# Kernel optimization log

Measured on AMD Instinct MI355X. Metric: run time of the kernel, lower is better.

The kernel has to match this reference:

```python
import jax, jax.numpy as jnp
import numpy as np

# Model dims (from MambaLayer: Mamba2(d_model=256, d_state=128, d_conv=4, expand=2, headdim=64))
D_MODEL = 256
D_INNER = 512
D_STATE = 128
NHEADS = 8
HEADDIM = 64
D_CONV = 4
CONV_DIM = D_INNER + 2 * D_STATE          # 768
D_IN_PROJ = 2 * D_INNER + 2 * D_STATE + NHEADS  # 1288
ATT_HEADS = 8
MLP_HID = 4 * D_MODEL
NUM_CLASSES = 2


def _mamba2(x, in_proj_w, conv_w, conv_b, dt_bias, A_log, D_param, norm_w, out_proj_w):
    """Mamba2 forward (SSD selective scan), ngroups=1, no in_proj/out_proj bias."""
    b, L, _ = x.shape
    zxbcdt = x @ in_proj_w.T                                   # (b,L,1288)
    z = zxbcdt[..., :D_INNER]                                   # gate
    xBC = zxbcdt[..., D_INNER:D_INNER + CONV_DIM]
    dt = jax.nn.softplus(zxbcdt[..., -NHEADS:] + dt_bias)       # (b,L,h)
    # depthwise causal conv1d (kernel 4) + SiLU
    xpad = jnp.pad(xBC, ((0, 0), (D_CONV - 1, 0), (0, 0)))
    xBC = sum(conv_w[:, k] * xpad[:, k:k + L, :] for k in range(D_CONV)) + conv_b
    xBC = jax.nn.silu(xBC)
    xs = xBC[..., :D_INNER].reshape(b, L, NHEADS, HEADDIM)      # (b,L,h,p)
    Bm = xBC[..., D_INNER:D_INNER + D_STATE]                    # (b,L,n)
    Cm = xBC[..., D_INNER + D_STATE:]                           # (b,L,n)
    dA = jnp.exp(dt * (-jnp.exp(A_log)))                        # (b,L,h)

    def step(h_prev, inp):
        dA_t, dt_t, B_t, C_t, x_t = inp                         # (b,h),(b,h),(b,n),(b,n),(b,h,p)
        h = h_prev * dA_t[..., None, None] + (dt_t[..., None] * x_t)[..., None] * B_t[:, None, None, :]
        return h, jnp.einsum('bhpn,bn->bhp', h, C_t)

    tfirst = lambda a: jnp.moveaxis(a, 1, 0)
    h0 = jnp.zeros((b, NHEADS, HEADDIM, D_STATE), x.dtype)
    _, ys = jax.lax.scan(step, h0, (tfirst(dA), tfirst(dt), tfirst(Bm), tfirst(Cm), tfirst(xs)))
    y = jnp.moveaxis(ys, 0, 1) + D_param[None, None, :, None] * xs
    # gated RMSNorm then out projection
    y = y.reshape(b, L, D_INNER) * jax.nn.silu(z)
    y = y * jax.lax.rsqrt(jnp.mean(y * y, -1, keepdims=True) + 1e-5) * norm_w
    return y @ out_proj_w.T


def _cross_attn(x, ctx, wq, wk, wv, wo, wo_b, w1, b1, ln_w, ln_b, w2, b2):
    """CrossModalAttention.forward: attn -> out_proj -> Mlp (no residual, per source)."""
    b, t, c = x.shape
    hd = c // ATT_HEADS
    heads = lambda a: a.reshape(b, -1, ATT_HEADS, hd).transpose(0, 2, 1, 3)
    q, k, v = heads(x @ wq.T), heads(ctx @ wk.T), heads(ctx @ wv.T)
    att = jax.nn.softmax(jnp.einsum('bhxd,bhyd->bhxy', q, k) * (hd ** -0.5), axis=-1)
    o = jnp.einsum('bhxy,bhyd->bhxd', att, v).transpose(0, 2, 1, 3).reshape(b, t, c)
    o = o @ wo.T + wo_b
    h = jax.nn.gelu(o @ w1.T + b1, approximate=False)
    mu = jnp.mean(h, -1, keepdims=True)
    var = jnp.mean((h - mu) ** 2, -1, keepdims=True)
    h = (h - mu) * jax.lax.rsqrt(var + 1e-5) * ln_w + ln_b
    return h @ w2.T + b2


def setup_inputs() -> dict:
    key = jax.random.key(0)
    ks = iter(jax.random.split(key, 32))
    f32 = jnp.float32
    w = lambda *s: jax.random.normal(next(ks), s, f32) * 0.02
    return {
        'x': jax.random.normal(next(ks), (2, 2048, D_MODEL), f32),
        'context': jax.random.normal(next(ks), (2, 2048, D_MODEL), f32),
        'in_proj_w': w(D_IN_PROJ, D_MODEL),
        'conv_w': w(CONV_DIM, D_CONV),
        'conv_b': jnp.zeros((CONV_DIM,), f32),
        'dt_bias': jax.random.normal(next(ks), (NHEADS,), f32) * 0.5,
        'A_log': jnp.log(jnp.linspace(1.0, 16.0, NHEADS).astype(f32)),
        'D_param': jnp.ones((NHEADS,), f32),
        'norm_w': jnp.ones((D_INNER,), f32),
        'out_proj_w': w(D_MODEL, D_INNER),
        'wq': w(D_MODEL, D_MODEL),
        'wk': w(D_MODEL, D_MODEL),
        'wv': w(D_MODEL, D_MODEL),
        'wo': w(D_MODEL, D_MODEL),
        'wo_b': jnp.zeros((D_MODEL,), f32),
        'w1': w(MLP_HID, D_MODEL),
        'b1': jnp.zeros((MLP_HID,), f32),
        'ln_w': jnp.ones((MLP_HID,), f32),
        'ln_b': jnp.zeros((MLP_HID,), f32),
        'w2': w(D_MODEL, MLP_HID),
        'b2': jnp.zeros((D_MODEL,), f32),
        'head_w': w(NUM_CLASSES, D_MODEL),
        'head_b': jnp.zeros((NUM_CLASSES,), f32),
    }


def reference(x, context, in_proj_w, conv_w, conv_b, dt_bias, A_log, D_param, norm_w, out_proj_w,
              wq, wk, wv, wo, wo_b, w1, b1, ln_w, ln_b, w2, b2, head_w, head_b):
    h = x + _mamba2(x, in_proj_w, conv_w, conv_b, dt_bias, A_log, D_param, norm_w, out_proj_w)
    h = _cross_attn(h, context, wq, wk, wv, wo, wo_b, w1, b1, ln_w, ln_b, w2, b2)
    # ClsHead: mean-pool over tokens, linear to classes
    return jnp.mean(h, axis=1) @ head_w.T + head_b
```

## Files before the change

### kernel.cpp

```cpp
#include <hip/hip_runtime.h>
#include <hip/hip_bf16.h>
#include <math.h>

#define DEVFN __device__ __forceinline__

constexpr int BATCH = 2;
constexpr int SEQ   = 2048;
constexpr int DM    = 256;
constexpr int DI    = 512;
constexpr int DSTATE= 128;
constexpr int NH    = 8;
constexpr int HD    = 64;
constexpr int CDIM  = 768;
constexpr int DPROJ = 1288;
constexpr int MTOK  = BATCH*SEQ;
constexpr int HID   = 1024;
constexpr int CHUNK = 32;
constexpr int NCHUNK= SEQ/CHUNK;
constexpr int NSPLIT= 4;
constexpr int KVLEN = SEQ/NSPLIT;

typedef __bf16 bf16x8 __attribute__((ext_vector_type(8)));
typedef __bf16 bf16x4 __attribute__((ext_vector_type(4)));
typedef float  f32x4  __attribute__((ext_vector_type(4)));

DEVFN float gelu_exact(float x){ return 0.5f*x*(1.f+erff(x*0.70710678118654752f)); }
DEVFN float silu_f(float x){ return x/(1.f+expf(-x)); }

DEVFN bf16x8 pack8(float4 a, float4 b){
  bf16x8 r;
  r[0]=(__bf16)a.x; r[1]=(__bf16)a.y; r[2]=(__bf16)a.z; r[3]=(__bf16)a.w;
  r[4]=(__bf16)b.x; r[5]=(__bf16)b.y; r[6]=(__bf16)b.z; r[7]=(__bf16)b.w;
  return r;
}
DEVFN f32x4 mfma16(bf16x8 a, bf16x8 b, f32x4 c){
  return __builtin_amdgcn_mfma_f32_16x16x32_bf16(a, b, c, 0, 0, 0);
}

__global__ __launch_bounds__(256)
void cvt_in(const float* __restrict__ x, const float* __restrict__ ctx,
            __bf16* __restrict__ xbf, __bf16* __restrict__ ctxbf)
{
  const int MN = MTOK*DM;
  int idx = (blockIdx.x*256 + threadIdx.x)*4;
  const float* src = (idx < MN) ? (x + idx) : (ctx + idx - MN);
  __bf16* dst = (idx < MN) ? (xbf + idx) : (ctxbf + idx - MN);
  float4 v = *(const float4*)src;
  bf16x4 o;
  o[0]=(__bf16)v.x; o[1]=(__bf16)v.y; o[2]=(__bf16)v.z; o[3]=(__bf16)v.w;
  *(bf16x4*)dst = o;
}

template<int ACT, bool HASBIAS>
__global__ __launch_bounds__(256)
void gemm128(const __bf16* __restrict__ A, const float* __restrict__ W,
             const float* __restrict__ bias, __bf16* __restrict__ C,
             int M, int N, int K)
{
  __shared__ __bf16 As[128][40];
  __shared__ __bf16 Ws[128][40];
  const int tid = threadIdx.x;
  const int bm = blockIdx.x * 128, bn = blockIdx.y * 128;
  const int wv = tid >> 6, lane = tid & 63;
  const int quad = lane >> 4, mr = lane & 15;
  const int wm = (wv >> 1) * 64, wn = (wv & 1) * 64;
  const int srow = tid >> 2;
  const int skc  = (tid & 3) * 8;

  const __bf16* ap0 = A + (size_t)(bm + srow)*K + skc;
  const __bf16* ap1 = A + (size_t)(bm + srow + 64)*K + skc;
  const bool wok0 = (bn + srow) < N;
  const bool wok1 = (bn + srow + 64) < N;
  const float* wp0 = W + (size_t)(bn + srow)*K + skc;
  const float* wp1 = W + (size_t)(bn + srow + 64)*K + skc;

  bf16x8 A0 = *(const bf16x8*)ap0;
  bf16x8 A1 = *(const bf16x8*)ap1;
  float4 z4 = make_float4(0,0,0,0);
  float4 W00 = wok0 ? *(const float4*)wp0     : z4;
  float4 W01 = wok0 ? *(const float4*)(wp0+4) : z4;
  float4 W10 = wok1 ? *(const float4*)wp1     : z4;
  float4 W11 = wok1 ? *(const float4*)(wp1+4) : z4;

  f32x4 acc[4][4];
  #pragma unroll
  for (int i=0;i<4;i++)
    #pragma unroll
    for (int j=0;j<4;j++) acc[i][j] = f32x4{0.f,0.f,0.f,0.f};

  for (int k0 = 0; k0 < K; k0 += 32) {
    __syncthreads();
    *(bf16x8*)&As[srow   ][skc] = A0;
    *(bf16x8*)&As[srow+64][skc] = A1;
    *(bf16x8*)&Ws[srow   ][skc] = pack8(W00, W01);
    *(bf16x8*)&Ws[srow+64][skc] = pack8(W10, W11);
    __syncthreads();
    if (k0 + 32 < K){
      int kn = k0 + 32;
      A0 = *(const bf16x8*)(ap0+kn);
      A1 = *(const bf16x8*)(ap1+kn);
      W00 = wok0 ? *(const float4*)(wp0+kn)   : z4;
      W01 = wok0 ? *(const float4*)(wp0+kn+4) : z4;
      W10 = wok1 ? *(const float4*)(wp1+kn)   : z4;
      W11 = wok1 ? *(const float4*)(wp1+kn+4) : z4;
    }
    bf16x8 af[4], bf[4];
    #pragma unroll
    for (int i=0;i<4;i++) af[i] = *(const bf16x8*)&As[wm + i*16 + mr][quad*8];
    #pragma unroll
    for (int j=0;j<4;j++) bf[j] = *(const bf16x8*)&Ws[wn + j*16 + mr][quad*8];
    #pragma unroll
    for (int i=0;i<4;i++)
      #pragma unroll
      for (int j=0;j<4;j++)
        acc[i][j] = mfma16(af[i], bf[j], acc[i][j]);
  }

  #pragma unroll
  for (int j=0;j<4;j++){
    int col = bn + wn + j*16 + mr;
    if (col >= N) continue;
    float bb = HASBIAS ? bias[col] : 0.f;
    #pragma unroll
    for (int i=0;i<4;i++){
      #pragma unroll
      for (int reg=0; reg<4; reg++){
        int row = bm + wm + i*16 + quad*4 + reg;
        float vv = acc[i][j][reg] + bb;
        if (ACT == 1) vv = gelu_exact(vv);
        C[(size_t)row*N + col] = (__bf16)vv;
      }
    }
  }
}

template<int EPI, bool HASBIAS, bool HASRES>
__global__ __launch_bounds__(256)
void gemm64d(const __bf16* __restrict__ A, const float* __restrict__ W,
             const float* __restrict__ bias, const __bf16* __restrict__ resid,
             float* __restrict__ Cf, __bf16* __restrict__ Cb,
             int M, int N, int K)
{
  __shared__ __bf16 As[64][40];
  __shared__ __bf16 Ws[64][40];
  const int tid = threadIdx.x;
  const int bm = blockIdx.x*64, bn = blockIdx.y*64;
  const int w = tid >> 6, lane = tid & 63;
  const int quad = lane >> 4, mr = lane & 15;
  const int wm = (w >> 1) * 32, wn = (w & 1) * 32;
  const int srow = tid >> 2, skc = (tid & 3) * 8;

  const __bf16* ap = A + (size_t)(bm + srow)*K + skc;
  const float*  wp = W + (size_t)(bn + srow)*K + skc;
  bf16x8 a0 = *(const bf16x8*)ap;
  float4 w0 = *(const float4*)wp, w1 = *(const float4*)(wp+4);

  f32x4 acc[2][2];
  #pragma unroll
  for (int i=0;i<2;i++)
    #pragma unroll
    for (int j=0;j<2;j++) acc[i][j] = f32x4{0.f,0.f,0.f,0.f};

  for (int k0 = 0; k0 < K; k0 += 32){
    __syncthreads();
    *(bf16x8*)&As[srow][skc] = a0;
    *(bf16x8*)&Ws[srow][skc] = pack8(w0, w1);
    __syncthreads();
    if (k0 + 32 < K){
      a0 = *(const bf16x8*)(ap+k0+32);
      w0 = *(const float4*)(wp+k0+32); w1 = *(const float4*)(wp+k0+36);
    }
    bf16x8 af[2], bfr[2];
    af[0]  = *(const bf16x8*)&As[wm      + mr][quad*8];
    af[1]  = *(const bf16x8*)&As[wm + 16 + mr][quad*8];
    bfr[0] = *(const bf16x8*)&Ws[wn      + mr][quad*8];
    bfr[1] = *(const bf16x8*)&Ws[wn + 16 + mr][quad*8];
    #pragma unroll
    for (int i=0;i<2;i++)
      #pragma unroll
      for (int j=0;j<2;j++)
        acc[i][j] = mfma16(af[i], bfr[j], acc[i][j]);
  }

  #pragma unroll
  for (int j=0;j<2;j++){
    int col = bn + wn + j*16 + mr;
    float bb = HASBIAS ? bias[col] : 0.f;
    #pragma unroll
    for (int i=0;i<2;i++)
      #pragma unroll
      for (int reg=0;reg<4;reg++){
        int row = bm + wm + i*16 + quad*4 + reg;
        float vv = acc[i][j][reg] + bb;
        if (HASRES) vv += (float)resid[(size_t)row*N + col];
        if (EPI == 0) Cf[(size_t)row*N + col] = vv;
        else          Cb[(size_t)row*N + col] = (__bf16)vv;
      }
  }
}

__global__ __launch_bounds__(256)
void qkv_gemm(const __bf16* __restrict__ hres, const __bf16* __restrict__ ctx,
              const float* __restrict__ wq, const float* __restrict__ wk,
              const float* __restrict__ wv, __bf16* __restrict__ qo,
              __bf16* __restrict__ ko, __bf16* __restrict__ vt)
{
  __shared__ __bf16 As[64][40];
  __shared__ __bf16 Ws[64][40];
  const int tid = threadIdx.x;
  const int bm = blockIdx.x*64, bn = blockIdx.y*64, z = blockIdx.z;
  const int K = DM, N = DM;
  const __bf16* A = (z == 0) ? hres : ctx;
  const float*  W = (z == 0) ? wq : (z == 1) ? wk : wv;
  const int w = tid >> 6, lane = tid & 63;
  const int quad = lane >> 4, mr = lane & 15;
  const int wm = (w >> 1) * 32, wn = (w & 1) * 32;
  const int srow = tid >> 2, skc = (tid & 3) * 8;

  const __bf16* ap = A + (size_t)(bm + srow)*K + skc;
  const float*  wp = W + (size_t)(bn + srow)*K + skc;
  bf16x8 a0 = *(const bf16x8*)ap;
  float4 w0 = *(const float4*)wp, w1 = *(const float4*)(wp+4);

  f32x4 acc[2][2];
  #pragma unroll
  for (int i=0;i<2;i++)
    #pragma unroll
    for (int j=0;j<2;j++) acc[i][j] = f32x4{0.f,0.f,0.f,0.f};

  for (int k0 = 0; k0 < K; k0 += 32){
    __syncthreads();
    *(bf16x8*)&As[srow][skc] = a0;
    *(bf16x8*)&Ws[srow][skc] = pack8(w0, w1);
    __syncthreads();
    if (k0 + 32 < K){
      a0 = *(const bf16x8*)(ap+k0+32);
      w0 = *(const float4*)(wp+k0+32); w1 = *(const float4*)(wp+k0+36);
    }
    bf16x8 af[2], bfr[2];
    af[0]  = *(const bf16x8*)&As[wm      + mr][quad*8];
    af[1]  = *(const bf16x8*)&As[wm + 16 + mr][quad*8];
    bfr[0] = *(const bf16x8*)&Ws[wn      + mr][quad*8];
    bfr[1] = *(const bf16x8*)&Ws[wn + 16 + mr][quad*8];
    #pragma unroll
    for (int i=0;i<2;i++)
      #pragma unroll
      for (int j=0;j<2;j++)
        acc[i][j] = mfma16(af[i], bfr[j], acc[i][j]);
  }

  if (z < 2){
    __bf16* C = (z == 0) ? qo : ko;
    #pragma unroll
    for (int j=0;j<2;j++){
      int col = bn + wn + j*16 + mr;
      #pragma unroll
      for (int i=0;i<2;i++)
        #pragma unroll
        for (int reg=0;reg<4;reg++){
          int row = bm + wm + i*16 + quad*4 + reg;
          C[(size_t)row*N + col] = (__bf16)acc[i][j][reg];
        }
    }
  } else {
    #pragma unroll
    for (int j=0;j<2;j++){
      int col = bn + wn + j*16 + mr;
      int h = col >> 5, dl = col & 31;
      #pragma unroll
      for (int i=0;i<2;i++){
        int rowb = bm + wm + i*16 + quad*4;
        int b = rowb >> 11, t = rowb & 2047;
        bf16x4 o;
        #pragma unroll
        for (int reg=0;reg<4;reg++) o[reg] = (__bf16)acc[i][j][reg];
        *(bf16x4*)(vt + ((size_t)(b*NH + h)*32 + dl)*SEQ + t) = o;
      }
    }
  }
}

__global__ __launch_bounds__(256)
void dtda_kernel(const __bf16* __restrict__ zx, const float* __restrict__ dt_bias,
                 const float* __restrict__ A_log, float* __restrict__ dtb,
                 float* __restrict__ ldab)
{
  int idx = blockIdx.x*256 + threadIdx.x;
  int t = idx & 2047, bh = idx >> 11;
  int b = bh >> 3, h = bh & 7;
  float raw = (float)zx[(size_t)(b*SEQ + t)*DPROJ + 2*DI + 2*DSTATE + h] + dt_bias[h];
  float dt = fmaxf(raw, 0.f) + log1pf(expf(-fabsf(raw)));
  dtb[idx]  = dt;
  ldab[idx] = -__expf(A_log[h]) * dt;
}

__global__ __launch_bounds__(256)
void conv_silu_kernel(const __bf16* __restrict__ zx, const float* __restrict__ convw,
                      const float* __restrict__ convb, __bf16* __restrict__ xBC)
{
  int idx = blockIdx.x*256 + threadIdx.x;
  int c = idx % CDIM;
  int bt = idx / CDIM;
  int b = bt >> 11, t = bt & 2047;
  float4 w4 = *(const float4*)(convw + c*4);
  const float* wp = (const float*)&w4;
  float acc = convb[c];
  #pragma unroll
  for (int k=0;k<4;k++){
    int ts = t - 3 + k;
    if (ts >= 0)
      acc = fmaf(wp[k], (float)zx[(size_t)(b*SEQ + ts)*DPROJ + DI + c], acc);
  }
  xBC[(size_t)bt*CDIM + c] = (__bf16)silu_f(acc);
}

__global__ __launch_bounds__(256)
void chunk_state(const __bf16* __restrict__ xBC, const float* __restrict__ dtb,
                 const float* __restrict__ ldab, __bf16* __restrict__ Hc,
                 float* __restrict__ Ac)
{
  const int blk = blockIdx.x;
  const int ch = blk & 63, bh = blk >> 6;
  const int b = bh >> 3, h = bh & 7;
  const int t0 = ch*CHUNK;
  const int tid = threadIdx.x;
  __shared__ float csS[CHUNK], wendS[CHUNK];
  __shared__ __bf16 Xw[64][40];
  __shared__ __bf16 Bt[128][40];

  if (tid < 32){
    float v  = ldab[bh*SEQ + t0 + tid];
    float dtv = dtb[bh*SEQ + t0 + tid];
    #pragma unroll
    for (int off=1; off<32; off<<=1){
      float o = __shfl_up(v, off, 32);
      if (tid >= off) v += o;
    }
    csS[tid] = v;
    float cs31 = __shfl(v, 31, 32);
    wendS[tid] = __expf(cs31 - v) * dtv;
  }
  __syncthreads();
  {
    int s  = tid >> 3;
    int pg = (tid & 7) * 8;
    bf16x8 xv = *(const bf16x8*)(xBC + (size_t)(b*SEQ + t0 + s)*CDIM + h*HD + pg);
    float wgt = wendS[s];
    #pragma unroll
    for (int e=0;e<8;e++) Xw[pg+e][s] = (__bf16)((float)xv[e] * wgt);
    int ng = (tid & 7) * 16;
    const __bf16* bp = xBC + (size_t)(b*SEQ + t0 + s)*CDIM + DI + ng;
    bf16x8 b0 = *(const bf16x8*)bp;
    bf16x8 b1 = *(const bf16x8*)(bp+8);
    #pragma unroll
    for (int e=0;e<8;e++){ Bt[ng+e][s] = b0[e]; Bt[ng+8+e][s] = b1[e]; }
  }
  if (tid == 0) Ac[blk] = __expf(csS[31]);
  __syncthreads();

  const int w = tid >> 6, lane = tid & 63, quad = lane >> 4, mr = lane & 15;
  bf16x8 af = *(const bf16x8*)&Xw[w*16 + mr][quad*8];
  __bf16* out = Hc + (size_t)blk*8192;
  #pragma unroll
  for (int j=0;j<8;j++){
    bf16x8 bfm = *(const bf16x8*)&Bt[j*16 + mr][quad*8];
    f32x4 a = mfma16(af, bfm, f32x4{0.f,0.f,0.f,0.f});
    #pragma unroll
    for (int reg=0; reg<4; reg++){
      int p = w*16 + quad*4 + reg;
      out[p*128 + j*16 + mr] = (__bf16)a[reg];
    }
  }
}

__global__ __launch_bounds__(256)
void state_prefix(__bf16* __restrict__ Hc, const float* __restrict__ Ac)
{
  const int blk = blockIdx.x;
  const int bh = blk >> 5, pp = blk & 31;
  const int tid = threadIdx.x;
  const int p = pp*2 + (tid >> 7), n = tid & 127;
  __shared__ float AcS[64];
  if (tid < 64) AcS[tid] = Ac[bh*64 + tid];
  __syncthreads();
  __bf16* base = Hc + (size_t)bh*64*8192 + p*128 + n;
  float run = 0.f;
  float v = (float)base[0];
  for (int c=0; c<64; c++){
    float vn = (c < 63) ? (float)base[(size_t)(c+1)*8192] : 0.f;
    base[(size_t)c*8192] = (__bf16)run;
    run = fmaf(AcS[c], run, v);
    v = vn;
  }
}

__global__ __launch_bounds__(256)
void chunk_out(const __bf16* __restrict__ xBC, const float* __restrict__ dtb,
               const float* __restrict__ ldab, const __bf16* __restrict__ h0buf,
               const float* __restrict__ Dparam, __bf16* __restrict__ ybuf)
{
  const int blk = blockIdx.x;
  const int ch = blk & 63, bh = blk >> 6;
  const int b = bh >> 3, h = bh & 7;
  const int t0 = ch*CHUNK;
  const int tid = threadIdx.x;
  __shared__ float csS[CHUNK], dtS[CHUNK];
  __shared__ __bf16 Xct[64][40];
  __shared__ __bf16 Ms[32][40];

  if (tid < 32){
    float v = ldab[bh*SEQ + t0 + tid];
    dtS[tid] = dtb[bh*SEQ + t0 + tid];
    #pragma unroll
    for (int off=1; off<32; off<<=1){
      float o = __shfl_up(v, off, 32);
      if (tid >= off) v += o;
    }
    csS[tid] = v;
  }
  __syncthreads();
  {
    int s  = tid >> 3;
    int pg = (tid & 7) * 8;
    bf16x8 xv = *(const bf16x8*)(xBC + (size_t)(b*SEQ + t0 + s)*CDIM + h*HD + pg);
    #pragma unroll
    for (int e=0;e<8;e++) Xct[pg+e][s] = xv[e];
  }

  const int w = tid >> 6, lane = tid & 63, quad = lane >> 4, mr = lane & 15;
  const int ti = w >> 1, si = w & 1;

  const __bf16* Crow = xBC + (size_t)(b*SEQ + t0 + ti*16 + mr)*CDIM + DI + DSTATE;
  bf16x8 af[4];
  #pragma unroll
  for (int kk=0; kk<4; kk++)
    af[kk] = *(const bf16x8*)(Crow + kk*32 + quad*8);
  f32x4 sacc = f32x4{0.f,0.f,0.f,0.f};
  const __bf16* Brow = xBC + (size_t)(b*SEQ + t0 + si*16 + mr)*CDIM + DI;
  #pragma unroll
  for (int kk=0; kk<4; kk++){
    bf16x8 bfm = *(const bf16x8*)(Brow + kk*32 + quad*8);
    sacc = mfma16(af[kk], bfm, sacc);
  }
  #pragma unroll
  for (int reg=0; reg<4; reg++){
    int t = ti*16 + quad*4 + reg;
    int s = si*16 + mr;
    float m = 0.f;
    if (s <= t) m = __expf(csS[t] - csS[s]) * dtS[s] * sacc[reg];
    Ms[t][s] = (__bf16)m;
  }
  __syncthreads();

  f32x4 acc[2] = { f32x4{0.f,0.f,0.f,0.f}, f32x4{0.f,0.f,0.f,0.f} };
  const __bf16* h0r = h0buf + (size_t)blk*8192;
  #pragma unroll
  for (int j=0;j<2;j++){
    int p = (si*2 + j)*16 + mr;
    #pragma unroll
    for (int kk=0; kk<4; kk++){
      bf16x8 bh0 = *(const bf16x8*)(h0r + (size_t)p*128 + kk*32 + quad*8);
      acc[j] = mfma16(af[kk], bh0, acc[j]);
    }
  }
  #pragma unroll
  for (int reg=0;reg<4;reg++){
    int t = ti*16 + quad*4 + reg;
    float e = __expf(csS[t]);
    acc[0][reg] *= e;
    acc[1][reg] *= e;
  }
  bf16x8 am = *(const bf16x8*)&Ms[ti*16 + mr][quad*8];
  #pragma unroll
  for (int j=0;j<2;j++){
    int p = (si*2 + j)*16 + mr;
    bf16x8 bx = *(const bf16x8*)&Xct[p][quad*8];
    acc[j] = mfma16(am, bx, acc[j]);
  }
  const float Dv = Dparam[h];
  #pragma unroll
  for (int j=0;j<2;j++){
    int p = (si*2 + j)*16 + mr;
    #pragma unroll
    for (int reg=0;reg<4;reg++){
      int t = t0 + ti*16 + quad*4 + reg;
      float xv = (float)xBC[(size_t)(b*SEQ + t)*CDIM + h*HD + p];
      ybuf[(size_t)(b*SEQ + t)*DI + h*HD + p] = (__bf16)fmaf(Dv, xv, acc[j][reg]);
    }
  }
}

__global__ __launch_bounds__(128)
void rmsgate_kernel(__bf16* __restrict__ y, const __bf16* __restrict__ zx,
                    const float* __restrict__ normw)
{
  const int row = blockIdx.x, tid = threadIdx.x;
  const __bf16* zrow = zx + (size_t)row*DPROJ;
  __bf16* yrow = y + (size_t)row*DI;
  bf16x4 yv = *(const bf16x4*)(yrow + tid*4);
  bf16x4 zv = *(const bf16x4*)(zrow + tid*4);
  float g[4];
  float ss = 0.f;
  #pragma unroll
  for (int e=0;e<4;e++){
    g[e] = (float)yv[e] * silu_f((float)zv[e]);
    ss += g[e]*g[e];
  }
  #pragma unroll
  for (int off=1; off<64; off<<=1) ss += __shfl_xor(ss, off);
  __shared__ float red[2];
  if ((tid & 63)==0) red[tid>>6] = ss;
  __syncthreads();
  float tot = red[0] + red[1];
  float rs = rsqrtf(tot * (1.f/DI) + 1e-5f);
  float4 nw = *(const float4*)(normw + tid*4);
  const float* nwp = (const float*)&nw;
  bf16x4 o;
  #pragma unroll
  for (int e=0;e<4;e++) o[e] = (__bf16)(g[e]*rs*nwp[e]);
  *(bf16x4*)(yrow + tid*4) = o;
}

__global__ __launch_bounds__(256)
void flash_part(const __bf16* __restrict__ qb, const __bf16* __restrict__ kb,
                const __bf16* __restrict__ vt, float* __restrict__ opart,
                float* __restrict__ lpart)
{
  const int qt = blockIdx.x, ksp = blockIdx.y, bh = blockIdx.z;
  const int b = bh >> 3, h = bh & 7;
  const int tid = threadIdx.x;
  const int w = tid >> 6, lane = tid & 63;
  const int quad = lane >> 4, mr = lane & 15;
  const int qrow0 = b*SEQ + qt*128 + w*32;
  const float SC = 0.17677669529663687f;
  __shared__ __bf16 Pq[4][32][72];

  bf16x8 bq[2];
  #pragma unroll
  for (int i2=0;i2<2;i2++)
    bq[i2] = *(const bf16x8*)(qb + (size_t)(qrow0 + i2*16 + mr)*DM + h*32 + quad*8);

  f32x4 accO[2][2];
  #pragma unroll
  for (int i=0;i<2;i++)
    #pragma unroll
    for (int j=0;j<2;j++) accO[i][j] = f32x4{0.f,0.f,0.f,0.f};
  float lacc[2] = {0.f, 0.f};

  for (int kt=0; kt<KVLEN/64; kt++){
    const int kbase = b*SEQ + ksp*KVLEN + kt*64;
    float tl[2] = {0.f, 0.f};
    #pragma unroll
    for (int ik=0; ik<4; ik++){
      bf16x8 ak = *(const bf16x8*)(kb + (size_t)(kbase + ik*16 + mr)*DM + h*32 + quad*8);
      #pragma unroll
      for (int jq=0; jq<2; jq++){
        f32x4 st = mfma16(ak, bq[jq], f32x4{0.f,0.f,0.f,0.f});
        bf16x4 e4;
        float sa = 0.f;
        #pragma unroll
        for (int reg=0; reg<4; reg++){
          float e = __expf(st[reg] * SC);
          sa += e;
          e4[reg] = (__bf16)e;
        }
        tl[jq] += sa;
        *(bf16x4*)&Pq[w][jq*16 + mr][ik*16 + quad*4] = e4;
      }
    }
    #pragma unroll
    for (int jq=0; jq<2; jq++){
      float v = tl[jq];
      v += __shfl_xor(v, 16);
      v += __shfl_xor(v, 32);
      lacc[jq] += v;
    }
    #pragma unroll
    for (int ks=0; ks<2; ks++){
      bf16x8 pa0 = *(const bf16x8*)&Pq[w][     mr][ks*32 + quad*8];
      bf16x8 pa1 = *(const bf16x8*)&Pq[w][16 + mr][ks*32 + quad*8];
      #pragma unroll
      for (int j2=0; j2<2; j2++){
        bf16x8 bv = *(const bf16x8*)(vt + ((size_t)bh*32 + j2*16 + mr)*SEQ
                        + ksp*KVLEN + kt*64 + ks*32 + quad*8);
        accO[0][j2] = mfma16(pa0, bv, accO[0][j2]);
        accO[1][j2] = mfma16(pa1, bv, accO[1][j2]);
      }
    }
  }

  #pragma unroll
  for (int i2=0;i2<2;i2++)
    #pragma unroll
    for (int j2=0;j2<2;j2++)
      #pragma unroll
      for (int reg=0;reg<4;reg++){
        int row = qrow0 + i2*16 + quad*4 + reg;
        opart[((size_t)ksp*MTOK + row)*DM + h*32 + j2*16 + mr] = accO[i2][j2][reg];
      }
  if (quad == 0){
    #pragma unroll
    for (int jq=0;jq<2;jq++)
      lpart[((size_t)ksp*16 + bh)*SEQ + (qt*128 + w*32 + jq*16 + mr)] = lacc[jq];
  }
}

__global__ __launch_bounds__(256)
void flash_combine(const float* __restrict__ opart, const float* __restrict__ lpart,
                   __bf16* __restrict__ o)
{
  int idx = blockIdx.x*256 + threadIdx.x;
  int row = idx >> 6, d4 = (idx & 63)*4;
  int h = d4 >> 5;
  int b = row >> 11, t = row & 2047;
  float sx=0.f, sy=0.f, sz=0.f, sw=0.f, lsum=0.f;
  #pragma unroll
  for (int s4=0; s4<NSPLIT; s4++){
    float4 vv = *(const float4*)(opart + ((size_t)s4*MTOK + row)*DM + d4);
    sx += vv.x; sy += vv.y; sz += vv.z; sw += vv.w;
    lsum += lpart[((size_t)s4*16 + b*8 + h)*SEQ + t];
  }
  float inv = 1.f / lsum;
  bf16x4 ov;
  ov[0]=(__bf16)(sx*inv); ov[1]=(__bf16)(sy*inv);
  ov[2]=(__bf16)(sz*inv); ov[3]=(__bf16)(sw*inv);
  *(bf16x4*)(o + (size_t)row*DM + d4) = ov;
}

__global__ __launch_bounds__(256)
void lnorm_kernel(__bf16* __restrict__ hb, const float* __restrict__ lnw,
                  const float* __restrict__ lnb)
{
  const int row = blockIdx.x, tid = threadIdx.x;
  __bf16* hr = hb + (size_t)row*HID;
  bf16x4 v4 = *(const bf16x4*)(hr + tid*4);
  float v[4];
  float sum = 0.f, sq = 0.f;
  #pragma unroll
  for (int e=0;e<4;e++){ v[e] = (float)v4[e]; sum += v[e]; sq += v[e]*v[e]; }
  #pragma unroll
  for (int off=1; off<64; off<<=1){ sum += __shfl_xor(sum,off); sq += __shfl_xor(sq,off); }
  __shared__ float s1[4], s2[4];
  int w = tid>>6;
  if ((tid & 63)==0){ s1[w]=sum; s2[w]=sq; }
  __syncthreads();
  sum = (s1[0]+s1[1])+(s1[2]+s1[3]);
  sq  = (s2[0]+s2[1])+(s2[2]+s2[3]);
  float mu = sum * (1.f/HID);
  float var = sq * (1.f/HID) - mu*mu;
  float rstd = rsqrtf(var + 1e-5f);
  float4 wv = *(const float4*)(lnw + tid*4);
  float4 bv = *(const float4*)(lnb + tid*4);
  const float* wp = (const float*)&wv;
  const float* bp = (const float*)&bv;
  bf16x4 o;
  #pragma unroll
  for (int e=0;e<4;e++) o[e] = (__bf16)((v[e]-mu)*rstd*wp[e] + bp[e]);
  *(bf16x4*)(hr + tid*4) = o;
}

__global__ __launch_bounds__(256)
void pool_partial(const float* __restrict__ h2, float* __restrict__ part)
{
  const int blk = blockIdx.x;
  const int b = blk >> 4, seg = blk & 15;
  const int tid = threadIdx.x;
  float s = 0.f;
  const float* base = h2 + ((size_t)b*SEQ + seg*128)*DM + tid;
  #pragma unroll 8
  for (int t=0; t<128; t++) s += base[(size_t)t*DM];
  part[((size_t)b*16 + seg)*DM + tid] = s;
}

__global__ __launch_bounds__(128)
void head_kernel(const float* __restrict__ part, const float* __restrict__ headw,
                 const float* __restrict__ headb, float* __restrict__ out)
{
  const int b = blockIdx.x;
  const int tid = threadIdx.x;
  __shared__ float pooled[DM];
  for (int c=tid; c<DM; c+=128){
    float s = 0.f;
    #pragma unroll
    for (int gidx=0; gidx<16; gidx++) s += part[((size_t)b*16 + gidx)*DM + c];
    pooled[c] = s * (1.f/SEQ);
  }
  __syncthreads();
  int cls = tid >> 6, lane = tid & 63;
  float acc = 0.f;
  for (int c=lane; c<DM; c+=64) acc += pooled[c]*headw[cls*DM + c];
  #pragma unroll
  for (int off=1; off<64; off<<=1) acc += __shfl_xor(acc, off);
  if (lane == 0) out[b*2 + cls] = acc + headb[cls];
}

extern "C" void kernel_launch(void* const* d_in, const int* in_sizes, int n_in,
                              void* d_out, int out_size, void* d_ws, size_t ws_size,
                              hipStream_t stream)
{
  const float* x         = (const float*)d_in[0];
  const float* context   = (const float*)d_in[1];
  const float* in_proj_w = (const float*)d_in[2];
  const float* conv_w    = (const float*)d_in[3];
  const float* conv_b    = (const float*)d_in[4];
  const float* dt_bias   = (const float*)d_in[5];
  const float* A_log     = (const float*)d_in[6];
  const float* D_param   = (const float*)d_in[7];
  const float* norm_w    = (const float*)d_in[8];
  const float* out_proj_w= (const float*)d_in[9];
  const float* wq  = (const float*)d_in[10];
  const float* wk  = (const float*)d_in[11];
  const float* wv  = (const float*)d_in[12];
  const float* wo  = (const float*)d_in[13];
  const float* wo_b= (const float*)d_in[14];
  const float* w1  = (const float*)d_in[15];
  const float* b1  = (const float*)d_in[16];
  const float* ln_w= (const float*)d_in[17];
  const float* ln_b= (const float*)d_in[18];
  const float* w2  = (const float*)d_in[19];
  const float* b2  = (const float*)d_in[20];
  const float* head_w = (const float*)d_in[21];
  const float* head_b = (const float*)d_in[22];
  float* out = (float*)d_out;
  float* ws  = (float*)d_ws;

  __bf16* xbf   = (__bf16*)ws;
  __bf16* ctxbf = (__bf16*)(ws + 524288);
  __bf16* zx    = (__bf16*)(ws + 1048576);
  __bf16* xBC   = (__bf16*)(ws + 3686400);
  float* dtb    = ws + 5259264;
  float* ldab   = ws + 5292032;
  __bf16* Hcb   = (__bf16*)(ws + 5324800);
  float* Acb    = ws + 9519104;
  __bf16* ybuf  = (__bf16*)(ws + 9520128);
  __bf16* hres  = (__bf16*)(ws + 10568704);
  __bf16* qbf   = (__bf16*)(ws + 11092992);
  __bf16* kbf   = (__bf16*)(ws + 11617280);
  __bf16* vtbf  = (__bf16*)(ws + 12141568);
  float* opart  = ws + 12665856;
  float* lpart  = ws + 16860160;
  __bf16* obf   = (__bf16*)(ws + 16991232);
  __bf16* o2bf  = (__bf16*)(ws + 17515520);
  __bf16* h1bf  = (__bf16*)(ws + 5324800);
  float* h2     = ws + 12665856;
  float* partb  = ws + 16860160;

  const dim3 g64(MTOK/64, DM/64);

  cvt_in<<<dim3(2*MTOK*DM/1024), dim3(256), 0, stream>>>(x, context, xbf, ctxbf);
  gemm128<0,false><<<dim3(MTOK/128, (DPROJ+127)/128), dim3(256), 0, stream>>>(
      xbf, in_proj_w, nullptr, zx, MTOK, DPROJ, DM);
  dtda_kernel<<<dim3(MTOK*NH/256), dim3(256), 0, stream>>>(zx, dt_bias, A_log, dtb, ldab);
  conv_silu_kernel<<<dim3(MTOK*CDIM/256), dim3(256), 0, stream>>>(
      zx, conv_w, conv_b, xBC);
  chunk_state<<<dim3(BATCH*NH*NCHUNK), dim3(256), 0, stream>>>(
      xBC, dtb, ldab, Hcb, Acb);
  state_prefix<<<dim3(BATCH*NH*32), dim3(256), 0, stream>>>(Hcb, Acb);
  chunk_out<<<dim3(BATCH*NH*NCHUNK), dim3(256), 0, stream>>>(
      xBC, dtb, ldab, Hcb, D_param, ybuf);
  rmsgate_kernel<<<dim3(MTOK), dim3(128), 0, stream>>>(ybuf, zx, norm_w);
  gemm64d<1,false,true><<<g64, dim3(256), 0, stream>>>(
      ybuf, out_proj_w, nullptr, xbf, nullptr, hres, MTOK, DM, DI);
  qkv_gemm<<<dim3(MTOK/64, DM/64, 3), dim3(256), 0, stream>>>(
      hres, ctxbf, wq, wk, wv, qbf, kbf, vtbf);
  flash_part<<<dim3(SEQ/128, NSPLIT, BATCH*NH), dim3(256), 0, stream>>>(
      qbf, kbf, vtbf, opart, lpart);
  flash_combine<<<dim3(MTOK*64/256), dim3(256), 0, stream>>>(opart, lpart, obf);
  gemm64d<1,true,false><<<g64, dim3(256), 0, stream>>>(
      obf, wo, wo_b, nullptr, nullptr, o2bf, MTOK, DM, DM);
  gemm128<1,true><<<dim3(MTOK/128, HID/128), dim3(256), 0, stream>>>(
      o2bf, w1, b1, h1bf, MTOK, HID, DM);
  lnorm_kernel<<<dim3(MTOK), dim3(256), 0, stream>>>(h1bf, ln_w, ln_b);
  gemm64d<0,true,false><<<g64, dim3(256), 0, stream>>>(
      h1bf, w2, b2, nullptr, h2, nullptr, MTOK, DM, HID);
  pool_partial<<<dim3(32), dim3(256), 0, stream>>>(h2, partb);
  head_kernel<<<dim3(BATCH), dim3(128), 0, stream>>>(partb, head_w, head_b, out);
  (void)in_sizes; (void)n_in; (void)out_size; (void)ws_size;
}
```

Before: 309.9 us.

## Fuse input conversion, dt, flash combine into neighbors; pool before final linear

```diff
diff --git a/kernel.cpp b/kernel.cpp
--- a/kernel.cpp
+++ b/kernel.cpp
@@ -22,6 +22,7 @@
 
 typedef __bf16 bf16x8 __attribute__((ext_vector_type(8)));
 typedef __bf16 bf16x4 __attribute__((ext_vector_type(4)));
+typedef __bf16 bf16x2 __attribute__((ext_vector_type(2)));
 typedef float  f32x4  __attribute__((ext_vector_type(4)));
 
 DEVFN float gelu_exact(float x){ return 0.5f*x*(1.f+erff(x*0.70710678118654752f)); }
@@ -37,23 +38,9 @@
   return __builtin_amdgcn_mfma_f32_16x16x32_bf16(a, b, c, 0, 0, 0);
 }
 
-__global__ __launch_bounds__(256)
-void cvt_in(const float* __restrict__ x, const float* __restrict__ ctx,
-            __bf16* __restrict__ xbf, __bf16* __restrict__ ctxbf)
-{
-  const int MN = MTOK*DM;
-  int idx = (blockIdx.x*256 + threadIdx.x)*4;
-  const float* src = (idx < MN) ? (x + idx) : (ctx + idx - MN);
-  __bf16* dst = (idx < MN) ? (xbf + idx) : (ctxbf + idx - MN);
-  float4 v = *(const float4*)src;
-  bf16x4 o;
-  o[0]=(__bf16)v.x; o[1]=(__bf16)v.y; o[2]=(__bf16)v.z; o[3]=(__bf16)v.w;
-  *(bf16x4*)dst = o;
-}
-
-template<int ACT, bool HASBIAS>
-__global__ __launch_bounds__(256)
-void gemm128(const __bf16* __restrict__ A, const float* __restrict__ W,
+template<int ACT, bool HASBIAS, bool AF32>
+__global__ __launch_bounds__(256)
+void gemm128(const void* __restrict__ Av, const float* __restrict__ W,
              const float* __restrict__ bias, __bf16* __restrict__ C,
              int M, int N, int K)
 {
@@ -67,15 +54,23 @@
   const int srow = tid >> 2;
   const int skc  = (tid & 3) * 8;
 
-  const __bf16* ap0 = A + (size_t)(bm + srow)*K + skc;
-  const __bf16* ap1 = A + (size_t)(bm + srow + 64)*K + skc;
+  const float*  af0 = (const float*)Av + (size_t)(bm + srow)*K + skc;
+  const float*  af1 = (const float*)Av + (size_t)(bm + srow + 64)*K + skc;
+  const __bf16* ab0 = (const __bf16*)Av + (size_t)(bm + srow)*K + skc;
+  const __bf16* ab1 = (const __bf16*)Av + (size_t)(bm + srow + 64)*K + skc;
   const bool wok0 = (bn + srow) < N;
   const bool wok1 = (bn + srow + 64) < N;
   const float* wp0 = W + (size_t)(bn + srow)*K + skc;
   const float* wp1 = W + (size_t)(bn + srow + 64)*K + skc;
 
-  bf16x8 A0 = *(const bf16x8*)ap0;
-  bf16x8 A1 = *(const bf16x8*)ap1;
+  bf16x8 A0, A1;
+  if (AF32){
+    A0 = pack8(*(const float4*)af0, *(const float4*)(af0+4));
+    A1 = pack8(*(const float4*)af1, *(const float4*)(af1+4));
+  } else {
+    A0 = *(const bf16x8*)ab0;
+    A1 = *(const bf16x8*)ab1;
+  }
   float4 z4 = make_float4(0,0,0,0);
   float4 W00 = wok0 ? *(const float4*)wp0     : z4;
   float4 W01 = wok0 ? *(const float4*)(wp0+4) : z4;
@@ -97,23 +92,28 @@
     __syncthreads();
     if (k0 + 32 < K){
       int kn = k0 + 32;
-      A0 = *(const bf16x8*)(ap0+kn);
-      A1 = *(const bf16x8*)(ap1+kn);
+      if (AF32){
+        A0 = pack8(*(const float4*)(af0+kn), *(const float4*)(af0+kn+4));
+        A1 = pack8(*(const float4*)(af1+kn), *(const float4*)(af1+kn+4));
+      } else {
+        A0 = *(const bf16x8*)(ab0+kn);
+        A1 = *(const bf16x8*)(ab1+kn);
+      }
       W00 = wok0 ? *(const float4*)(wp0+kn)   : z4;
       W01 = wok0 ? *(const float4*)(wp0+kn+4) : z4;
       W10 = wok1 ? *(const float4*)(wp1+kn)   : z4;
       W11 = wok1 ? *(const float4*)(wp1+kn+4) : z4;
     }
-    bf16x8 af[4], bf[4];
-    #pragma unroll
-    for (int i=0;i<4;i++) af[i] = *(const bf16x8*)&As[wm + i*16 + mr][quad*8];
-    #pragma unroll
-    for (int j=0;j<4;j++) bf[j] = *(const bf16x8*)&Ws[wn + j*16 + mr][quad*8];
+    bf16x8 afr[4], bfr[4];
+    #pragma unroll
+    for (int i=0;i<4;i++) afr[i] = *(const bf16x8*)&As[wm + i*16 + mr][quad*8];
+    #pragma unroll
+    for (int j=0;j<4;j++) bfr[j] = *(const bf16x8*)&Ws[wn + j*16 + mr][quad*8];
     #pragma unroll
     for (int i=0;i<4;i++)
       #pragma unroll
       for (int j=0;j<4;j++)
-        acc[i][j] = mfma16(af[i], bf[j], acc[i][j]);
+        acc[i][j] = mfma16(afr[i], bfr[j], acc[i][j]);
   }
 
   #pragma unroll
@@ -134,12 +134,10 @@
   }
 }
 
-template<int EPI, bool HASBIAS, bool HASRES>
-__global__ __launch_bounds__(256)
-void gemm64d(const __bf16* __restrict__ A, const float* __restrict__ W,
-             const float* __restrict__ bias, const __bf16* __restrict__ resid,
-             float* __restrict__ Cf, __bf16* __restrict__ Cb,
-             int M, int N, int K)
+__global__ __launch_bounds__(256)
+void gemm_outproj(const __bf16* __restrict__ A, const float* __restrict__ W,
+                  const float* __restrict__ residf, __bf16* __restrict__ Cb,
+                  int M, int N, int K)
 {
   __shared__ __bf16 As[64][40];
   __shared__ __bf16 Ws[64][40];
@@ -185,22 +183,19 @@
   #pragma unroll
   for (int j=0;j<2;j++){
     int col = bn + wn + j*16 + mr;
-    float bb = HASBIAS ? bias[col] : 0.f;
     #pragma unroll
     for (int i=0;i<2;i++)
       #pragma unroll
       for (int reg=0;reg<4;reg++){
         int row = bm + wm + i*16 + quad*4 + reg;
-        float vv = acc[i][j][reg] + bb;
-        if (HASRES) vv += (float)resid[(size_t)row*N + col];
-        if (EPI == 0) Cf[(size_t)row*N + col] = vv;
-        else          Cb[(size_t)row*N + col] = (__bf16)vv;
+        float vv = acc[i][j][reg] + residf[(size_t)row*N + col];
+        Cb[(size_t)row*N + col] = (__bf16)vv;
       }
   }
 }
 
 __global__ __launch_bounds__(256)
-void qkv_gemm(const __bf16* __restrict__ hres, const __bf16* __restrict__ ctx,
+void qkv_gemm(const __bf16* __restrict__ hres, const float* __restrict__ ctx,
               const float* __restrict__ wq, const float* __restrict__ wk,
               const float* __restrict__ wv, __bf16* __restrict__ qo,
               __bf16* __restrict__ ko, __bf16* __restrict__ vt)
@@ -210,16 +205,19 @@
   const int tid = threadIdx.x;
   const int bm = blockIdx.x*64, bn = blockIdx.y*64, z = blockIdx.z;
   const int K = DM, N = DM;
-  const __bf16* A = (z == 0) ? hres : ctx;
+  const bool abf = (z == 0);
   const float*  W = (z == 0) ? wq : (z == 1) ? wk : wv;
   const int w = tid >> 6, lane = tid & 63;
   const int quad = lane >> 4, mr = lane & 15;
   const int wm = (w >> 1) * 32, wn = (w & 1) * 32;
   const int srow = tid >> 2, skc = (tid & 3) * 8;
 
-  const __bf16* ap = A + (size_t)(bm + srow)*K + skc;
-  const float*  wp = W + (size_t)(bn + srow)*K + skc;
-  bf16x8 a0 = *(const bf16x8*)ap;
+  const __bf16* apb = hres + (size_t)(bm + srow)*K + skc;
+  const float*  apf = ctx  + (size_t)(bm + srow)*K + skc;
+  const float*  wp  = W + (size_t)(bn + srow)*K + skc;
+  bf16x8 a0;
+  if (abf) a0 = *(const bf16x8*)apb;
+  else     a0 = pack8(*(const float4*)apf, *(const float4*)(apf+4));
   float4 w0 = *(const float4*)wp, w1 = *(const float4*)(wp+4);
 
   f32x4 acc[2][2];
@@ -234,7 +232,8 @@
     *(bf16x8*)&Ws[srow][skc] = pack8(w0, w1);
     __syncthreads();
     if (k0 + 32 < K){
-      a0 = *(const bf16x8*)(ap+k0+32);
+      if (abf) a0 = *(const bf16x8*)(apb+k0+32);
+      else     a0 = pack8(*(const float4*)(apf+k0+32), *(const float4*)(apf+k0+36));
       w0 = *(const float4*)(wp+k0+32); w1 = *(const float4*)(wp+k0+36);
     }
     bf16x8 af[2], bfr[2];
@@ -281,22 +280,89 @@
 }
 
 __global__ __launch_bounds__(256)
-void dtda_kernel(const __bf16* __restrict__ zx, const float* __restrict__ dt_bias,
-                 const float* __restrict__ A_log, float* __restrict__ dtb,
-                 float* __restrict__ ldab)
-{
-  int idx = blockIdx.x*256 + threadIdx.x;
-  int t = idx & 2047, bh = idx >> 11;
-  int b = bh >> 3, h = bh & 7;
-  float raw = (float)zx[(size_t)(b*SEQ + t)*DPROJ + 2*DI + 2*DSTATE + h] + dt_bias[h];
-  float dt = fmaxf(raw, 0.f) + log1pf(expf(-fabsf(raw)));
-  dtb[idx]  = dt;
-  ldab[idx] = -__expf(A_log[h]) * dt;
-}
-
-__global__ __launch_bounds__(256)
-void conv_silu_kernel(const __bf16* __restrict__ zx, const float* __restrict__ convw,
-                      const float* __restrict__ convb, __bf16* __restrict__ xBC)
+void wo_gemm(const float* __restrict__ opart, const float* __restrict__ lpart,
+             const float* __restrict__ W, const float* __restrict__ bias,
+             __bf16* __restrict__ Cb)
+{
+  __shared__ __bf16 As[64][40];
+  __shared__ __bf16 Ws[64][40];
+  const int tid = threadIdx.x;
+  const int bm = blockIdx.x*64, bn = blockIdx.y*64;
+  const int K = DM, N = DM;
+  const int w = tid >> 6, lane = tid & 63;
+  const int quad = lane >> 4, mr = lane & 15;
+  const int wm = (w >> 1) * 32, wn = (w & 1) * 32;
+  const int srow = tid >> 2, skc = (tid & 3) * 8;
+
+  const int row = bm + srow;
+  const int b = row >> 11, t = row & 2047;
+  const float* wp = W + (size_t)(bn + srow)*K + skc;
+
+  f32x4 acc[2][2];
+  #pragma unroll
+  for (int i=0;i<2;i++)
+    #pragma unroll
+    for (int j=0;j<2;j++) acc[i][j] = f32x4{0.f,0.f,0.f,0.f};
+
+  for (int k0 = 0; k0 < K; k0 += 32){
+    __syncthreads();
+    {
+      int col = k0 + skc;
+      int h = col >> 5;
+      float lsum = 0.f;
+      #pragma unroll
+      for (int s=0;s<NSPLIT;s++)
+        lsum += lpart[((size_t)s*16 + b*8 + h)*SEQ + t];
+      float inv = 1.f / lsum;
+      float va[8] = {0,0,0,0,0,0,0,0};
+      #pragma unroll
+      for (int s=0;s<NSPLIT;s++){
+        const float* op = opart + ((size_t)s*MTOK + row)*DM + col;
+        float4 u0 = *(const float4*)op;
+        float4 u1 = *(const float4*)(op+4);
+        va[0]+=u0.x; va[1]+=u0.y; va[2]+=u0.z; va[3]+=u0.w;
+        va[4]+=u1.x; va[5]+=u1.y; va[6]+=u1.z; va[7]+=u1.w;
+      }
+      bf16x8 a;
+      #pragma unroll
+      for (int e=0;e<8;e++) a[e] = (__bf16)(va[e]*inv);
+      *(bf16x8*)&As[srow][skc] = a;
+      float4 w0 = *(const float4*)(wp+k0);
+      float4 w1 = *(const float4*)(wp+k0+4);
+      *(bf16x8*)&Ws[srow][skc] = pack8(w0, w1);
+    }
+    __syncthreads();
+    bf16x8 af[2], bfr[2];
+    af[0]  = *(const bf16x8*)&As[wm      + mr][quad*8];
+    af[1]  = *(const bf16x8*)&As[wm + 16 + mr][quad*8];
+    bfr[0] = *(const bf16x8*)&Ws[wn      + mr][quad*8];
+    bfr[1] = *(const bf16x8*)&Ws[wn + 16 + mr][quad*8];
+    #pragma unroll
+    for (int i=0;i<2;i++)
+      #pragma unroll
+      for (int j=0;j<2;j++)
+        acc[i][j] = mfma16(af[i], bfr[j], acc[i][j]);
+  }
+
+  #pragma unroll
+  for (int j=0;j<2;j++){
+    int col = bn + wn + j*16 + mr;
+    float bb = bias[col];
+    #pragma unroll
+    for (int i=0;i<2;i++)
+      #pragma unroll
+      for (int reg=0;reg<4;reg++){
+        int r2 = bm + wm + i*16 + quad*4 + reg;
+        Cb[(size_t)r2*N + col] = (__bf16)(acc[i][j][reg] + bb);
+      }
+  }
+}
+
+__global__ __launch_bounds__(256)
+void conv_dt_kernel(const __bf16* __restrict__ zx, const float* __restrict__ convw,
+                    const float* __restrict__ convb, const float* __restrict__ dt_bias,
+                    const float* __restrict__ A_log, __bf16* __restrict__ xBC,
+                    float* __restrict__ dtb, float* __restrict__ ldab)
 {
   int idx = blockIdx.x*256 + threadIdx.x;
   int c = idx % CDIM;
@@ -312,6 +378,13 @@
       acc = fmaf(wp[k], (float)zx[(size_t)(b*SEQ + ts)*DPROJ + DI + c], acc);
   }
   xBC[(size_t)bt*CDIM + c] = (__bf16)silu_f(acc);
+  if (c < NH){
+    float raw = (float)zx[(size_t)bt*DPROJ + 2*DI + 2*DSTATE + c] + dt_bias[c];
+    float dt = fmaxf(raw, 0.f) + log1pf(expf(-fabsf(raw)));
+    int o = (b*NH + c)*SEQ + t;
+    dtb[o]  = dt;
+    ldab[o] = -__expf(A_log[c]) * dt;
+  }
 }
 
 __global__ __launch_bounds__(256)
@@ -377,20 +450,24 @@
 void state_prefix(__bf16* __restrict__ Hc, const float* __restrict__ Ac)
 {
   const int blk = blockIdx.x;
-  const int bh = blk >> 5, pp = blk & 31;
+  const int bh = blk >> 4, sub = blk & 15;
   const int tid = threadIdx.x;
-  const int p = pp*2 + (tid >> 7), n = tid & 127;
+  const int off = sub*512 + tid*2;
   __shared__ float AcS[64];
   if (tid < 64) AcS[tid] = Ac[bh*64 + tid];
+  __bf16* base = Hc + (size_t)bh*64*8192 + off;
+  bf16x2 v[64];
+  #pragma unroll
+  for (int c=0;c<64;c++) v[c] = *(const bf16x2*)(base + (size_t)c*8192);
   __syncthreads();
-  __bf16* base = Hc + (size_t)bh*64*8192 + p*128 + n;
-  float run = 0.f;
-  float v = (float)base[0];
-  for (int c=0; c<64; c++){
-    float vn = (c < 63) ? (float)base[(size_t)(c+1)*8192] : 0.f;
-    base[(size_t)c*8192] = (__bf16)run;
-    run = fmaf(AcS[c], run, v);
-    v = vn;
+  float r0 = 0.f, r1 = 0.f;
+  #pragma unroll
+  for (int c=0;c<64;c++){
+    bf16x2 o; o[0] = (__bf16)r0; o[1] = (__bf16)r1;
+    *(bf16x2*)(base + (size_t)c*8192) = o;
+    float a = AcS[c];
+    r0 = fmaf(a, r0, (float)v[c][0]);
+    r1 = fmaf(a, r1, (float)v[c][1]);
   }
 }
 
@@ -603,28 +680,6 @@
     for (int jq=0;jq<2;jq++)
       lpart[((size_t)ksp*16 + bh)*SEQ + (qt*128 + w*32 + jq*16 + mr)] = lacc[jq];
   }
-}
-
-__global__ __launch_bounds__(256)
-void flash_combine(const float* __restrict__ opart, const float* __restrict__ lpart,
-                   __bf16* __restrict__ o)
-{
-  int idx = blockIdx.x*256 + threadIdx.x;
-  int row = idx >> 6, d4 = (idx & 63)*4;
-  int h = d4 >> 5;
-  int b = row >> 11, t = row & 2047;
-  float sx=0.f, sy=0.f, sz=0.f, sw=0.f, lsum=0.f;
-  #pragma unroll
-  for (int s4=0; s4<NSPLIT; s4++){
-    float4 vv = *(const float4*)(opart + ((size_t)s4*MTOK + row)*DM + d4);
-    sx += vv.x; sy += vv.y; sz += vv.z; sw += vv.w;
-    lsum += lpart[((size_t)s4*16 + b*8 + h)*SEQ + t];
-  }
-  float inv = 1.f / lsum;
-  bf16x4 ov;
-  ov[0]=(__bf16)(sx*inv); ov[1]=(__bf16)(sy*inv);
-  ov[2]=(__bf16)(sz*inv); ov[3]=(__bf16)(sw*inv);
-  *(bf16x4*)(o + (size_t)row*DM + d4) = ov;
 }
 
 __global__ __launch_bounds__(256)
@@ -660,38 +715,62 @@
 }
 
 __global__ __launch_bounds__(256)
-void pool_partial(const float* __restrict__ h2, float* __restrict__ part)
+void pool_ln(const __bf16* __restrict__ h1, float* __restrict__ pp)
 {
   const int blk = blockIdx.x;
-  const int b = blk >> 4, seg = blk & 15;
+  const int b = blk >> 6, seg = blk & 63;
   const int tid = threadIdx.x;
-  float s = 0.f;
-  const float* base = h2 + ((size_t)b*SEQ + seg*128)*DM + tid;
-  #pragma unroll 8
-  for (int t=0; t<128; t++) s += base[(size_t)t*DM];
-  part[((size_t)b*16 + seg)*DM + tid] = s;
-}
-
-__global__ __launch_bounds__(128)
-void head_kernel(const float* __restrict__ part, const float* __restrict__ headw,
-                 const float* __restrict__ headb, float* __restrict__ out)
-{
-  const int b = blockIdx.x;
-  const int tid = threadIdx.x;
-  __shared__ float pooled[DM];
-  for (int c=tid; c<DM; c+=128){
-    float s = 0.f;
-    #pragma unroll
-    for (int gidx=0; gidx<16; gidx++) s += part[((size_t)b*16 + gidx)*DM + c];
-    pooled[c] = s * (1.f/SEQ);
+  const int c4 = tid*4;
+  float4 s = make_float4(0,0,0,0);
+  const __bf16* basep = h1 + ((size_t)(b*SEQ + seg*32))*HID + c4;
+  #pragma unroll 4
+  for (int r=0;r<32;r++){
+    bf16x4 v = *(const bf16x4*)(basep + (size_t)r*HID);
+    s.x += (float)v[0]; s.y += (float)v[1]; s.z += (float)v[2]; s.w += (float)v[3];
+  }
+  *(float4*)(pp + ((size_t)(b*64+seg))*HID + c4) = s;
+}
+
+__global__ __launch_bounds__(256)
+void head2_kernel(const float* __restrict__ pp, const float* __restrict__ w2,
+                  const float* __restrict__ b2, const float* __restrict__ hw,
+                  const float* __restrict__ hb, float* __restrict__ out)
+{
+  const int b = blockIdx.x, tid = threadIdx.x;
+  __shared__ float pooled[HID];
+  __shared__ float w2h[DM];
+  {
+    int c4 = tid*4;
+    float4 s = make_float4(0,0,0,0);
+    #pragma unroll 4
+    for (int seg=0;seg<64;seg++){
+      float4 v = *(const float4*)(pp + ((size_t)(b*64+seg))*HID + c4);
+      s.x+=v.x; s.y+=v.y; s.z+=v.z; s.w+=v.w;
+    }
+    const float inv = 1.f/(float)SEQ;
+    *(float4*)&pooled[c4] = make_float4(s.x*inv, s.y*inv, s.z*inv, s.w*inv);
   }
   __syncthreads();
-  int cls = tid >> 6, lane = tid & 63;
-  float acc = 0.f;
-  for (int c=lane; c<DM; c+=64) acc += pooled[c]*headw[cls*DM + c];
-  #pragma unroll
-  for (int off=1; off<64; off<<=1) acc += __shfl_xor(acc, off);
-  if (lane == 0) out[b*2 + cls] = acc + headb[cls];
+  {
+    float acc = 0.f;
+    const float* wr = w2 + (size_t)tid*HID;
+    #pragma unroll 8
+    for (int k=0;k<HID;k+=4){
+      float4 wv4 = *(const float4*)(wr+k);
+      float4 pv  = *(const float4*)&pooled[k];
+      acc += wv4.x*pv.x + wv4.y*pv.y + wv4.z*pv.z + wv4.w*pv.w;
+    }
+    w2h[tid] = acc + b2[tid];
+  }
+  __syncthreads();
+  if (tid < 128){
+    int cls = tid >> 6, lane = tid & 63;
+    float acc = 0.f;
+    for (int c=lane;c<DM;c+=64) acc += w2h[c]*hw[cls*DM+c];
+    #pragma unroll
+    for (int off=1;off<64;off<<=1) acc += __shfl_xor(acc, off);
+    if (lane == 0) out[b*2 + cls] = acc + hb[cls];
+  }
 }
 
 extern "C" void kernel_launch(void* const* d_in, const int* in_sizes, int n_in,
@@ -724,56 +803,47 @@
   float* out = (float*)d_out;
   float* ws  = (float*)d_ws;
 
-  __bf16* xbf   = (__bf16*)ws;
-  __bf16* ctxbf = (__bf16*)(ws + 524288);
-  __bf16* zx    = (__bf16*)(ws + 1048576);
-  __bf16* xBC   = (__bf16*)(ws + 3686400);
-  float* dtb    = ws + 5259264;
-  float* ldab   = ws + 5292032;
-  __bf16* Hcb   = (__bf16*)(ws + 5324800);
-  float* Acb    = ws + 9519104;
-  __bf16* ybuf  = (__bf16*)(ws + 9520128);
-  __bf16* hres  = (__bf16*)(ws + 10568704);
-  __bf16* qbf   = (__bf16*)(ws + 11092992);
-  __bf16* kbf   = (__bf16*)(ws + 11617280);
-  __bf16* vtbf  = (__bf16*)(ws + 12141568);
-  float* opart  = ws + 12665856;
-  float* lpart  = ws + 16860160;
-  __bf16* obf   = (__bf16*)(ws + 16991232);
-  __bf16* o2bf  = (__bf16*)(ws + 17515520);
-  __bf16* h1bf  = (__bf16*)(ws + 5324800);
-  float* h2     = ws + 12665856;
-  float* partb  = ws + 16860160;
+  __bf16* zx    = (__bf16*)ws;
+  __bf16* xBC   = (__bf16*)(ws + 2637824);
+  float* dtb    = ws + 4210688;
+  float* ldab   = ws + 4243456;
+  __bf16* Hcb   = (__bf16*)(ws + 4276224);
+  float* Acb    = ws + 8470528;
+  __bf16* ybuf  = (__bf16*)(ws + 8471552);
+  __bf16* hres  = (__bf16*)(ws + 9520128);
+  __bf16* qbf   = (__bf16*)(ws + 10044416);
+  __bf16* kbf   = (__bf16*)(ws + 10568704);
+  __bf16* vtbf  = (__bf16*)(ws + 11092992);
+  float* opart  = ws + 11617280;
+  float* lpart  = ws + 15811584;
+  __bf16* o2bf  = (__bf16*)(ws + 15942656);
+  __bf16* h1bf  = (__bf16*)(ws + 4276224);
+  float* poolp  = ws + 11617280;
 
   const dim3 g64(MTOK/64, DM/64);
 
-  cvt_in<<<dim3(2*MTOK*DM/1024), dim3(256), 0, stream>>>(x, context, xbf, ctxbf);
-  gemm128<0,false><<<dim3(MTOK/128, (DPROJ+127)/128), dim3(256), 0, stream>>>(
-      xbf, in_proj_w, nullptr, zx, MTOK, DPROJ, DM);
-  dtda_kernel<<<dim3(MTOK*NH/256), dim3(256), 0, stream>>>(zx, dt_bias, A_log, dtb, ldab);
-  conv_silu_kernel<<<dim3(MTOK*CDIM/256), dim3(256), 0, stream>>>(
-      zx, conv_w, conv_b, xBC);
+  gemm128<0,false,true><<<dim3(MTOK/128, (DPROJ+127)/128), dim3(256), 0, stream>>>(
+      x, in_proj_w, nullptr, zx, MTOK, DPROJ, DM);
+  conv_dt_kernel<<<dim3(MTOK*CDIM/256), dim3(256), 0, stream>>>(
+      zx, conv_w, conv_b, dt_bias, A_log, xBC, dtb, ldab);
   chunk_state<<<dim3(BATCH*NH*NCHUNK), dim3(256), 0, stream>>>(
       xBC, dtb, ldab, Hcb, Acb);
-  state_prefix<<<dim3(BATCH*NH*32), dim3(256), 0, stream>>>(Hcb, Acb);
+  state_prefix<<<dim3(256), dim3(256), 0, stream>>>(Hcb, Acb);
   chunk_out<<<dim3(BATCH*NH*NCHUNK), dim3(256), 0, stream>>>(
       xBC, dtb, ldab, Hcb, D_param, ybuf);
   rmsgate_kernel<<<dim3(MTOK), dim3(128), 0, stream>>>(ybuf, zx, norm_w);
-  gemm64d<1,false,true><<<g64, dim3(256), 0, stream>>>(
-      ybuf, out_proj_w, nullptr, xbf, nullptr, hres, MTOK, DM, DI);
+  gemm_outproj<<<g64, dim3(256), 0, stream>>>(
+      ybuf, out_proj_w, x, hres, MTOK, DM, DI);
   qkv_gemm<<<dim3(MTOK/64, DM/64, 3), dim3(256), 0, stream>>>(
-      hres, ctxbf, wq, wk, wv, qbf, kbf, vtbf);
+      hres, context, wq, wk, wv, qbf, kbf, vtbf);
   flash_part<<<dim3(SEQ/128, NSPLIT, BATCH*NH), dim3(256), 0, stream>>>(
       qbf, kbf, vtbf, opart, lpart);
-  flash_combine<<<dim3(MTOK*64/256), dim3(256), 0, stream>>>(opart, lpart, obf);
-  gemm64d<1,true,false><<<g64, dim3(256), 0, stream>>>(
-      obf, wo, wo_b, nullptr, nullptr, o2bf, MTOK, DM, DM);
-  gemm128<1,true><<<dim3(MTOK/128, HID/128), dim3(256), 0, stream>>>(
+  wo_gemm<<<g64, dim3(256), 0, stream>>>(opart, lpart, wo, wo_b, o2bf);
+  gemm128<1,true,false><<<dim3(MTOK/128, HID/128), dim3(256), 0, stream>>>(
       o2bf, w1, b1, h1bf, MTOK, HID, DM);
   lnorm_kernel<<<dim3(MTOK), dim3(256), 0, stream>>>(h1bf, ln_w, ln_b);
-  gemm64d<0,true,false><<<g64, dim3(256), 0, stream>>>(
-      h1bf, w2, b2, nullptr, h2, nullptr, MTOK, DM, HID);
-  pool_partial<<<dim3(32), dim3(256), 0, stream>>>(h2, partb);
-  head_kernel<<<dim3(BATCH), dim3(128), 0, stream>>>(partb, head_w, head_b, out);
+  pool_ln<<<dim3(128), dim3(256), 0, stream>>>(h1bf, poolp);
+  head2_kernel<<<dim3(BATCH), dim3(256), 0, stream>>>(
+      poolp, w2, b2, head_w, head_b, out);
   (void)in_sizes; (void)n_in; (void)out_size; (void)ws_size;
 }
```

After: 320.6 us. 1.03x slower.
